# Kernel tuning notes

Measured on AMD Instinct MI355X. Metric: run time of the kernel, lower is better.

Reference implementation:

```python
import jax, jax.numpy as jnp
import numpy as np

T = 50000   # tuple nodes
N = 5000    # base-graph nodes (scatter-mean output size)
E = 800000  # edges per tuple relation
F_IN = 4652
DIM = 256
N_CLASSES = 5


def _lin_init(k, fan_in, fan_out):
    s = 1.0 / np.sqrt(fan_in)
    kw, kb = jax.random.split(k)
    W = jax.random.uniform(kw, (fan_in, fan_out), jnp.float32, -s, s)
    b = jax.random.uniform(kb, (fan_out,), jnp.float32, -s, s)
    return W, b


def setup_inputs() -> dict:
    key = jax.random.key(0)
    ks = jax.random.split(key, 24)
    inp = {}
    inp['x'] = jax.random.normal(ks[0], (T, F_IN), jnp.float32)
    inp['edge_index_1'] = jax.random.randint(ks[1], (2, E), 0, T, jnp.int32)
    inp['edge_index_2'] = jax.random.randint(ks[2], (2, E), 0, T, jnp.int32)
    inp['index_1'] = jax.random.randint(ks[3], (T,), 0, N, jnp.int32)
    inp['index_2'] = jax.random.randint(ks[4], (T,), 0, N, jnp.int32)
    # mlp_init: 4652 -> 256 -> 256
    inp['W_i1'], inp['b_i1'] = _lin_init(ks[5], F_IN, DIM)
    inp['W_i2'], inp['b_i2'] = _lin_init(ks[6], DIM, DIM)
    # GCN convs (PyG GCNConv: weight [in,out], bias [out])
    inp['Wc11'], inp['bc11'] = _lin_init(ks[7], DIM, DIM)
    inp['Wc12'], inp['bc12'] = _lin_init(ks[8], DIM, DIM)
    inp['Wc21'], inp['bc21'] = _lin_init(ks[9], DIM, DIM)
    inp['Wc22'], inp['bc22'] = _lin_init(ks[10], DIM, DIM)
    # mlp_1, mlp_2: 512 -> 256 -> 256
    inp['W_m1a'], inp['b_m1a'] = _lin_init(ks[11], 2 * DIM, DIM)
    inp['W_m1b'], inp['b_m1b'] = _lin_init(ks[12], DIM, DIM)
    inp['W_m2a'], inp['b_m2a'] = _lin_init(ks[13], 2 * DIM, DIM)
    inp['W_m2b'], inp['b_m2b'] = _lin_init(ks[14], DIM, DIM)
    # final mlp: 512 -> 256 -> 5
    inp['W_fa'], inp['b_fa'] = _lin_init(ks[15], 2 * DIM, DIM)
    inp['W_fb'], inp['b_fb'] = _lin_init(ks[16], DIM, N_CLASSES)
    return inp


def _gcn(x, src, dst, W, b):
    # PyG GCNConv default: add self-loops, symmetric deg^-1/2 normalization.
    n = x.shape[0]
    loop = jnp.arange(n, dtype=src.dtype)
    src = jnp.concatenate([src, loop])
    dst = jnp.concatenate([dst, loop])
    deg = jax.ops.segment_sum(jnp.ones_like(dst, x.dtype), dst, num_segments=n)
    dinv = jnp.where(deg > 0, jax.lax.rsqrt(deg), 0.0)
    norm = dinv[src] * dinv[dst]  # [E+n]
    h = x @ W                      # [n, dim]
    agg = jax.ops.segment_sum(h[src] * norm[:, None], dst, num_segments=n)
    return agg + b


def _mlp(x, Wa, ba, Wb, bb):
    return jax.nn.relu(x @ Wa + ba) @ Wb + bb


def _scatter_mean(x, idx, num_segments):
    s = jax.ops.segment_sum(x, idx, num_segments=num_segments)
    c = jax.ops.segment_sum(jnp.ones_like(idx, x.dtype), idx, num_segments=num_segments)
    return s / jnp.maximum(c, 1.0)[:, None]


def reference(x, edge_index_1, edge_index_2, index_1, index_2,
              W_i1, b_i1, W_i2, b_i2,
              Wc11, bc11, Wc12, bc12, Wc21, bc21, Wc22, bc22,
              W_m1a, b_m1a, W_m1b, b_m1b,
              W_m2a, b_m2a, W_m2b, b_m2b,
              W_fa, b_fa, W_fb, b_fb):
    s1, d1 = edge_index_1[0], edge_index_1[1]
    s2, d2 = edge_index_2[0], edge_index_2[1]
    h = _mlp(x, W_i1, b_i1, W_i2, b_i2)
    h1 = jax.nn.relu(_gcn(h, s1, d1, Wc11, bc11))
    h2 = jax.nn.relu(_gcn(h, s2, d2, Wc12, bc12))
    h = _mlp(jnp.concatenate([h1, h2], axis=-1), W_m1a, b_m1a, W_m1b, b_m1b)
    h1 = jax.nn.relu(_gcn(h, s1, d1, Wc21, bc21))
    h2 = jax.nn.relu(_gcn(h, s2, d2, Wc22, bc22))
    h = _mlp(jnp.concatenate([h1, h2], axis=-1), W_m2a, b_m2a, W_m2b, b_m2b)
    r1 = _scatter_mean(h, index_1, N)
    r2 = _scatter_mean(h, index_2, N)
    logits = _mlp(jnp.concatenate([r1, r2], axis=-1), W_fa, b_fa, W_fb, b_fb)
    return jax.nn.log_softmax(logits, axis=1)
```

## Files before the change

### kernel.cpp

```cpp
#include <hip/hip_runtime.h>
#include <hip/hip_bf16.h>

#define T_N 50000
#define N_N 5000
#define E_N 800000
#define FIN 4652
#define KP1 4672
#define DIM 256

typedef __bf16 bf16;
typedef __bf16 bf16x8 __attribute__((ext_vector_type(8)));
typedef float f32x4 __attribute__((ext_vector_type(4)));
typedef unsigned int u32;
typedef __attribute__((address_space(1))) const u32 gu32;
typedef __attribute__((address_space(3))) u32 lu32;

__global__ void prep_w_k(const float* __restrict__ W, bf16* __restrict__ Wt,
                         int K, int Kpad) {
  int k = blockIdx.x;
  int n = threadIdx.x;
  float v = (k < K) ? W[(size_t)k * DIM + n] : 0.f;
  Wt[(size_t)n * Kpad + k] = (bf16)v;
}

__global__ void hist_k(const int* __restrict__ bins, int* __restrict__ cnt, int n) {
  int i = blockIdx.x * 256 + threadIdx.x;
  if (i < n) atomicAdd(&cnt[bins[i]], 1);
}

__global__ void dinv_k(const int* __restrict__ cnt, float* __restrict__ dinv, int n) {
  int i = blockIdx.x * 256 + threadIdx.x;
  if (i < n) dinv[i] = rsqrtf((float)(cnt[i] + 1));
}

__global__ void scan_k(const int* __restrict__ cnt, int* __restrict__ offs,
                       int* __restrict__ curs, int n) {
  __shared__ int wsum[16];
  __shared__ int carry_s;
  int tid = threadIdx.x, wv = tid >> 6, ln = tid & 63;
  if (tid == 0) carry_s = 0;
  __syncthreads();
  for (int base = 0; base < n; base += 1024) {
    int i = base + tid;
    int v = (i < n) ? cnt[i] : 0;
    int s = v;
#pragma unroll
    for (int off = 1; off < 64; off <<= 1) {
      int t = __shfl_up(s, off);
      if (ln >= off) s += t;
    }
    if (ln == 63) wsum[wv] = s;
    __syncthreads();
    if (wv == 0) {
      int w = (ln < 16) ? wsum[ln] : 0;
#pragma unroll
      for (int off = 1; off < 16; off <<= 1) {
        int t = __shfl_up(w, off);
        if (ln >= off) w += t;
      }
      if (ln < 16) wsum[ln] = w;
    }
    __syncthreads();
    int woff = (wv == 0) ? 0 : wsum[wv - 1];
    int total = wsum[15];
    int excl = carry_s + woff + (s - v);
    if (i < n) { offs[i] = excl; curs[i] = excl; }
    __syncthreads();
    if (tid == 0) carry_s += total;
    __syncthreads();
  }
}

__global__ void scatter_k(const int* __restrict__ bins, const int* __restrict__ payload,
                          int* __restrict__ curs, int* __restrict__ out, int n) {
  int i = blockIdx.x * 256 + threadIdx.x;
  if (i < n) {
    int p = atomicAdd(&curs[bins[i]], 1);
    out[p] = payload ? payload[i] : i;
  }
}

__global__ __launch_bounds__(256) void gcn_agg_k(
    const bf16* __restrict__ P, const int* __restrict__ offs,
    const int* __restrict__ cnt, const int* __restrict__ ssrc,
    const float* __restrict__ dinv, const float* __restrict__ bias,
    bf16* __restrict__ HC, int col_off) {
  __shared__ float red[8][256];
  int i = blockIdx.x;
  int tid = threadIdx.x, g = tid >> 5, l = tid & 31;
  float di = dinv[i];
  float acc[8];
#pragma unroll
  for (int j = 0; j < 8; j++) acc[j] = 0.f;
  if (g == 0) {
    bf16x8 v = *(const bf16x8*)(P + (size_t)i * DIM + l * 8);
    float w = di * di;
#pragma unroll
    for (int j = 0; j < 8; j++) acc[j] += (float)v[j] * w;
  }
  int s0 = offs[i], e1 = s0 + cnt[i];
  for (int e = s0 + g; e < e1; e += 8) {
    int s = ssrc[e];
    float w = dinv[s] * di;
    bf16x8 v = *(const bf16x8*)(P + (size_t)s * DIM + l * 8);
#pragma unroll
    for (int j = 0; j < 8; j++) acc[j] += (float)v[j] * w;
  }
#pragma unroll
  for (int j = 0; j < 8; j++) red[g][l * 8 + j] = acc[j];
  __syncthreads();
  float r = 0.f;
#pragma unroll
  for (int gg = 0; gg < 8; gg++) r += red[gg][tid];
  float v = r + bias[tid];
  HC[(size_t)i * 512 + col_off + tid] = (bf16)fmaxf(v, 0.f);
}

__global__ __launch_bounds__(256) void mean_agg_k(
    const bf16* __restrict__ Hf, const int* __restrict__ offs,
    const int* __restrict__ cnt, const int* __restrict__ ids,
    bf16* __restrict__ RC, int col_off) {
  __shared__ float red[8][256];
  int nb = blockIdx.x;
  int tid = threadIdx.x, g = tid >> 5, l = tid & 31;
  int s0 = offs[nb], c = cnt[nb];
  float acc[8];
#pragma unroll
  for (int j = 0; j < 8; j++) acc[j] = 0.f;
  for (int e = s0 + g; e < s0 + c; e += 8) {
    int t = ids[e];
    bf16x8 v = *(const bf16x8*)(Hf + (size_t)t * DIM + l * 8);
#pragma unroll
    for (int j = 0; j < 8; j++) acc[j] += (float)v[j];
  }
#pragma unroll
  for (int j = 0; j < 8; j++) red[g][l * 8 + j] = acc[j];
  __syncthreads();
  float r = 0.f;
#pragma unroll
  for (int gg = 0; gg < 8; gg++) r += red[gg][tid];
  float denom = (c > 0) ? (float)c : 1.f;
  RC[(size_t)nb * 512 + col_off + tid] = (bf16)(r / denom);
}

template <int K>
__global__ __launch_bounds__(256) void gemm_b_k(
    const bf16* __restrict__ A, const bf16* __restrict__ Wt,
    const float* __restrict__ bias, bf16* __restrict__ C,
    int M, int relu) {
  constexpr int RB = K * 2;
  constexpr int RSH = (K == 256) ? 9 : 10;
  constexpr int NC = (64 * RB) / 1024;
  __shared__ __align__(16) char As[64 * RB];
  int tid = threadIdx.x;
  int wv = tid >> 6, ln = tid & 63;
  int q = ln >> 4, r16 = ln & 15;
  int bm = blockIdx.x * 64;
  const char* Ab = (const char*)(A + (size_t)bm * K);
  for (int c = wv; c < NC; c += 4) {
    int lo = c * 1024;
    int t = lo + ln * 16;
    int row = t >> RSH;
    int src = t ^ ((row & 7) << 4);
    __builtin_amdgcn_global_load_lds((gu32*)(Ab + src), (lu32*)(As + lo), 16, 0, 0);
  }
  __syncthreads();

  const bf16* Bp = Wt + (size_t)(wv * 64 + r16) * K + q * 8;
  f32x4 acc[4][4];
#pragma unroll
  for (int i = 0; i < 4; i++)
#pragma unroll
    for (int j = 0; j < 4; j++) acc[i][j] = f32x4{0.f, 0.f, 0.f, 0.f};

  int abase[4], axor[4];
#pragma unroll
  for (int mi = 0; mi < 4; mi++) {
    int row = mi * 16 + r16;
    abase[mi] = row * RB + q * 16;
    axor[mi] = (row & 7) << 4;
  }
#pragma unroll 2
  for (int k0 = 0; k0 < K; k0 += 32) {
    bf16x8 af[4], bv[4];
#pragma unroll
    for (int mi = 0; mi < 4; mi++)
      af[mi] = *(const bf16x8*)(As + ((abase[mi] + k0 * 2) ^ axor[mi]));
#pragma unroll
    for (int ni = 0; ni < 4; ni++)
      bv[ni] = *(const bf16x8*)(Bp + (size_t)ni * 16 * K + k0);
#pragma unroll
    for (int mi = 0; mi < 4; mi++)
#pragma unroll
      for (int ni = 0; ni < 4; ni++)
        acc[mi][ni] = __builtin_amdgcn_mfma_f32_16x16x32_bf16(af[mi], bv[ni], acc[mi][ni], 0, 0, 0);
  }
#pragma unroll
  for (int ni = 0; ni < 4; ni++) {
    int ng = wv * 64 + ni * 16 + r16;
    float bvv = bias ? bias[ng] : 0.f;
#pragma unroll
    for (int mi = 0; mi < 4; mi++) {
#pragma unroll
      for (int rr = 0; rr < 4; rr++) {
        int mg = bm + mi * 16 + q * 4 + rr;
        if (mg < M) {
          float vv = acc[mi][ni][rr] + bvv;
          if (relu) vv = fmaxf(vv, 0.f);
          C[(size_t)mg * DIM + ng] = (bf16)vv;
        }
      }
    }
  }
}

#define LDA 40

__device__ __forceinline__ void load_x8(const float* __restrict__ Xp, int kg, float* f) {
  if (kg + 8 <= FIN) {
    float4 u0 = *(const float4*)(Xp + kg);
    float4 u1 = *(const float4*)(Xp + kg + 4);
    f[0] = u0.x; f[1] = u0.y; f[2] = u0.z; f[3] = u0.w;
    f[4] = u1.x; f[5] = u1.y; f[6] = u1.z; f[7] = u1.w;
  } else {
#pragma unroll
    for (int j = 0; j < 8; j++) f[j] = (kg + j < FIN) ? Xp[kg + j] : 0.f;
  }
}

__global__ __launch_bounds__(256) void gemm_x_k(
    const float* __restrict__ X, const bf16* __restrict__ Wt,
    const float* __restrict__ bias, bf16* __restrict__ C) {
  __shared__ __align__(16) bf16 As[2][64 * LDA];
  int tid = threadIdx.x;
  int wv = tid >> 6, ln = tid & 63;
  int q = ln >> 4, r16 = ln & 15;
  int bm = blockIdx.x * 64;
  int ar = tid >> 2, acol = (tid & 3) * 8;
  int arow = bm + ar; if (arow > T_N - 1) arow = T_N - 1;
  const float* Xp = X + (size_t)arow * FIN;
  const bf16* Bp = Wt + (size_t)(wv * 64 + r16) * KP1 + q * 8;
  f32x4 acc[4][4];
#pragma unroll
  for (int i = 0; i < 4; i++)
#pragma unroll
    for (int j = 0; j < 4; j++) acc[i][j] = f32x4{0.f, 0.f, 0.f, 0.f};

  {
    float f0[8];
    load_x8(Xp, acol, f0);
    bf16x8 av;
#pragma unroll
    for (int j = 0; j < 8; j++) av[j] = (bf16)f0[j];
    *(bf16x8*)&As[0][ar * LDA + acol] = av;
  }
  __syncthreads();
  int cur = 0;
  for (int k0 = 0; k0 < KP1; k0 += 32) {
    float fn[8];
    int have = (k0 + 32 < KP1);
    if (have) load_x8(Xp, k0 + 32 + acol, fn);
    bf16x8 af[4], bv[4];
#pragma unroll
    for (int mi = 0; mi < 4; mi++)
      af[mi] = *(const bf16x8*)&As[cur][(mi * 16 + r16) * LDA + q * 8];
#pragma unroll
    for (int ni = 0; ni < 4; ni++)
      bv[ni] = *(const bf16x8*)(Bp + (size_t)ni * 16 * KP1 + k0);
#pragma unroll
    for (int mi = 0; mi < 4; mi++)
#pragma unroll
      for (int ni = 0; ni < 4; ni++)
        acc[mi][ni] = __builtin_amdgcn_mfma_f32_16x16x32_bf16(af[mi], bv[ni], acc[mi][ni], 0, 0, 0);
    if (have) {
      bf16x8 av;
#pragma unroll
      for (int j = 0; j < 8; j++) av[j] = (bf16)fn[j];
      *(bf16x8*)&As[cur ^ 1][ar * LDA + acol] = av;
    }
    __syncthreads();
    cur ^= 1;
  }
#pragma unroll
  for (int ni = 0; ni < 4; ni++) {
    int ng = wv * 64 + ni * 16 + r16;
    float bv2 = bias[ng];
#pragma unroll
    for (int mi = 0; mi < 4; mi++) {
#pragma unroll
      for (int rr = 0; rr < 4; rr++) {
        int mg = bm + mi * 16 + q * 4 + rr;
        if (mg < T_N) {
          float v = fmaxf(acc[mi][ni][rr] + bv2, 0.f);
          C[(size_t)mg * DIM + ng] = (bf16)v;
        }
      }
    }
  }
}

__global__ void final_k(const bf16* __restrict__ F1, const float* __restrict__ Wfb,
                        const float* __restrict__ bfb, float* __restrict__ out) {
  int i = blockIdx.x, l = threadIdx.x;
  float p[5] = {0.f, 0.f, 0.f, 0.f, 0.f};
  for (int k = l; k < DIM; k += 64) {
    float v = (float)F1[(size_t)i * DIM + k];
#pragma unroll
    for (int c = 0; c < 5; c++) p[c] += v * Wfb[k * 5 + c];
  }
#pragma unroll
  for (int off = 32; off > 0; off >>= 1)
#pragma unroll
    for (int c = 0; c < 5; c++) p[c] += __shfl_down(p[c], off);
  if (l == 0) {
    float z[5], m = -1e30f;
#pragma unroll
    for (int c = 0; c < 5; c++) { z[c] = p[c] + bfb[c]; m = fmaxf(m, z[c]); }
    float s = 0.f;
#pragma unroll
    for (int c = 0; c < 5; c++) s += expf(z[c] - m);
    float ls = m + logf(s);
#pragma unroll
    for (int c = 0; c < 5; c++) out[(size_t)i * 5 + c] = z[c] - ls;
  }
}

extern "C" void kernel_launch(void* const* d_in, const int* in_sizes, int n_in,
                              void* d_out, int out_size, void* d_ws, size_t ws_size,
                              hipStream_t stream) {
  (void)in_sizes; (void)out_size; (void)ws_size;
  if (n_in < 29) return;
  const float* x    = (const float*)d_in[0];
  const int* ei1    = (const int*)d_in[1];
  const int* ei2    = (const int*)d_in[2];
  const int* idx1   = (const int*)d_in[3];
  const int* idx2   = (const int*)d_in[4];
  const float* W_i1 = (const float*)d_in[5];  const float* b_i1 = (const float*)d_in[6];
  const float* W_i2 = (const float*)d_in[7];  const float* b_i2 = (const float*)d_in[8];
  const float* Wc11 = (const float*)d_in[9];  const float* bc11 = (const float*)d_in[10];
  const float* Wc12 = (const float*)d_in[11]; const float* bc12 = (const float*)d_in[12];
  const float* Wc21 = (const float*)d_in[13]; const float* bc21 = (const float*)d_in[14];
  const float* Wc22 = (const float*)d_in[15]; const float* bc22 = (const float*)d_in[16];
  const float* Wm1a = (const float*)d_in[17]; const float* bm1a = (const float*)d_in[18];
  const float* Wm1b = (const float*)d_in[19]; const float* bm1b = (const float*)d_in[20];
  const float* Wm2a = (const float*)d_in[21]; const float* bm2a = (const float*)d_in[22];
  const float* Wm2b = (const float*)d_in[23]; const float* bm2b = (const float*)d_in[24];
  const float* Wfa  = (const float*)d_in[25]; const float* bfa  = (const float*)d_in[26];
  const float* Wfb  = (const float*)d_in[27]; const float* bfb  = (const float*)d_in[28];

  char* base = (char*)d_ws;
  size_t off = 0;
  auto alloc = [&](size_t bytes) -> void* {
    off = (off + 255) & ~(size_t)255;
    void* p = base + off;
    off += bytes;
    return p;
  };

  bf16* WtI1  = (bf16*)alloc((size_t)DIM * KP1 * 2);
  bf16* WtI2  = (bf16*)alloc((size_t)DIM * 256 * 2);
  bf16* WtC11 = (bf16*)alloc((size_t)DIM * 256 * 2);
  bf16* WtC12 = (bf16*)alloc((size_t)DIM * 256 * 2);
  bf16* WtC21 = (bf16*)alloc((size_t)DIM * 256 * 2);
  bf16* WtC22 = (bf16*)alloc((size_t)DIM * 256 * 2);
  bf16* WtM1a = (bf16*)alloc((size_t)DIM * 512 * 2);
  bf16* WtM1b = (bf16*)alloc((size_t)DIM * 256 * 2);
  bf16* WtM2a = (bf16*)alloc((size_t)DIM * 512 * 2);
  bf16* WtM2b = (bf16*)alloc((size_t)DIM * 256 * 2);
  bf16* WtFa  = (bf16*)alloc((size_t)DIM * 512 * 2);

  int* cnt1   = (int*)alloc((size_t)T_N * 4);
  int* cnt2   = (int*)alloc((size_t)T_N * 4);
  int* cntN1  = (int*)alloc((size_t)N_N * 4);
  int* cntN2  = (int*)alloc((size_t)N_N * 4);
  int* offs1  = (int*)alloc((size_t)T_N * 4);
  int* curs1  = (int*)alloc((size_t)T_N * 4);
  int* offs2  = (int*)alloc((size_t)T_N * 4);
  int* curs2  = (int*)alloc((size_t)T_N * 4);
  int* offsN1 = (int*)alloc((size_t)N_N * 4);
  int* cursN1 = (int*)alloc((size_t)N_N * 4);
  int* offsN2 = (int*)alloc((size_t)N_N * 4);
  int* cursN2 = (int*)alloc((size_t)N_N * 4);
  float* dinv1 = (float*)alloc((size_t)T_N * 4);
  float* dinv2 = (float*)alloc((size_t)T_N * 4);
  int* sorted1 = (int*)alloc((size_t)E_N * 4);
  int* sorted2 = (int*)alloc((size_t)E_N * 4);
  int* sortedN1 = (int*)alloc((size_t)T_N * 4);
  int* sortedN2 = (int*)alloc((size_t)T_N * 4);
  bf16* SB0 = (bf16*)alloc((size_t)T_N * DIM * 2);
  bf16* SB1 = (bf16*)alloc((size_t)T_N * DIM * 2);
  bf16* SB2 = (bf16*)alloc((size_t)T_N * 512 * 2);
  bf16* RC  = (bf16*)alloc((size_t)N_N * 512 * 2);
  bf16* F1  = (bf16*)alloc((size_t)N_N * DIM * 2);
  float* out = (float*)d_out;

  hipMemsetAsync(cnt1, 0, (size_t)((char*)cntN2 + (size_t)N_N * 4 - (char*)cnt1), stream);

  prep_w_k<<<KP1, 256, 0, stream>>>(W_i1, WtI1, FIN, KP1);
  prep_w_k<<<256, 256, 0, stream>>>(W_i2, WtI2, 256, 256);
  prep_w_k<<<256, 256, 0, stream>>>(Wc11, WtC11, 256, 256);
  prep_w_k<<<256, 256, 0, stream>>>(Wc12, WtC12, 256, 256);
  prep_w_k<<<256, 256, 0, stream>>>(Wc21, WtC21, 256, 256);
  prep_w_k<<<256, 256, 0, stream>>>(Wc22, WtC22, 256, 256);
  prep_w_k<<<512, 256, 0, stream>>>(Wm1a, WtM1a, 512, 512);
  prep_w_k<<<256, 256, 0, stream>>>(Wm1b, WtM1b, 256, 256);
  prep_w_k<<<512, 256, 0, stream>>>(Wm2a, WtM2a, 512, 512);
  prep_w_k<<<256, 256, 0, stream>>>(Wm2b, WtM2b, 256, 256);
  prep_w_k<<<512, 256, 0, stream>>>(Wfa, WtFa, 512, 512);

  const int GE = (E_N + 255) / 256, GT = (T_N + 255) / 256;
  hist_k<<<GE, 256, 0, stream>>>(ei1 + E_N, cnt1, E_N);
  hist_k<<<GE, 256, 0, stream>>>(ei2 + E_N, cnt2, E_N);
  hist_k<<<GT, 256, 0, stream>>>(idx1, cntN1, T_N);
  hist_k<<<GT, 256, 0, stream>>>(idx2, cntN2, T_N);
  dinv_k<<<GT, 256, 0, stream>>>(cnt1, dinv1, T_N);
  dinv_k<<<GT, 256, 0, stream>>>(cnt2, dinv2, T_N);
  scan_k<<<1, 1024, 0, stream>>>(cnt1, offs1, curs1, T_N);
  scan_k<<<1, 1024, 0, stream>>>(cnt2, offs2, curs2, T_N);
  scan_k<<<1, 1024, 0, stream>>>(cntN1, offsN1, cursN1, N_N);
  scan_k<<<1, 1024, 0, stream>>>(cntN2, offsN2, cursN2, N_N);
  scatter_k<<<GE, 256, 0, stream>>>(ei1 + E_N, ei1, curs1, sorted1, E_N);
  scatter_k<<<GE, 256, 0, stream>>>(ei2 + E_N, ei2, curs2, sorted2, E_N);
  scatter_k<<<GT, 256, 0, stream>>>(idx1, nullptr, cursN1, sortedN1, T_N);
  scatter_k<<<GT, 256, 0, stream>>>(idx2, nullptr, cursN2, sortedN2, T_N);

  const int GM = (T_N + 63) / 64;
  const int GMn = (N_N + 63) / 64;
  gemm_x_k<<<GM, 256, 0, stream>>>(x, WtI1, b_i1, SB0);
  gemm_b_k<256><<<GM, 256, 0, stream>>>(SB0, WtI2, b_i2, SB1, T_N, 0);
  gemm_b_k<256><<<GM, 256, 0, stream>>>(SB1, WtC11, nullptr, SB0, T_N, 0);
  gcn_agg_k<<<T_N, 256, 0, stream>>>(SB0, offs1, cnt1, sorted1, dinv1, bc11, SB2, 0);
  gemm_b_k<256><<<GM, 256, 0, stream>>>(SB1, WtC12, nullptr, SB0, T_N, 0);
  gcn_agg_k<<<T_N, 256, 0, stream>>>(SB0, offs2, cnt2, sorted2, dinv2, bc12, SB2, 256);
  gemm_b_k<512><<<GM, 256, 0, stream>>>(SB2, WtM1a, bm1a, SB1, T_N, 1);
  gemm_b_k<256><<<GM, 256, 0, stream>>>(SB1, WtM1b, bm1b, SB0, T_N, 0);
  gemm_b_k<256><<<GM, 256, 0, stream>>>(SB0, WtC21, nullptr, SB1, T_N, 0);
  gcn_agg_k<<<T_N, 256, 0, stream>>>(SB1, offs1, cnt1, sorted1, dinv1, bc21, SB2, 0);
  gemm_b_k<256><<<GM, 256, 0, stream>>>(SB0, WtC22, nullptr, SB1, T_N, 0);
  gcn_agg_k<<<T_N, 256, 0, stream>>>(SB1, offs2, cnt2, sorted2, dinv2, bc22, SB2, 256);
  gemm_b_k<512><<<GM, 256, 0, stream>>>(SB2, WtM2a, bm2a, SB0, T_N, 1);
  gemm_b_k<256><<<GM, 256, 0, stream>>>(SB0, WtM2b, bm2b, SB1, T_N, 0);
  mean_agg_k<<<N_N, 256, 0, stream>>>(SB1, offsN1, cntN1, sortedN1, RC, 0);
  mean_agg_k<<<N_N, 256, 0, stream>>>(SB1, offsN2, cntN2, sortedN2, RC, 256);
  gemm_b_k<512><<<GMn, 256, 0, stream>>>(RC, WtFa, bfa, F1, N_N, 1);
  final_k<<<N_N, 64, 0, stream>>>(F1, Wfb, bfb, out);
}
```

Baseline: 2.729 ms.

## Batch preprocessing launches and merge paired GCN GEMMs and aggregations

Merges the eleven weight-transpose launches, the four histogram, four scan and four scatter launches into single batched kernels, and folds the dinv computation into the scan. The two per-relation GCN projections now run as one 512-wide GEMM with concatenated weights. The two aggregations and the two scatter-means each become one launch over a 2D grid. This cuts launch count and re-reads of the shared input activation. It adds an extra T×512 buffer and changes the GEMM block size to 512 threads.

```diff
diff --git a/kernel.cpp b/kernel.cpp
--- a/kernel.cpp
+++ b/kernel.cpp
@@ -15,34 +15,55 @@
 typedef __attribute__((address_space(1))) const u32 gu32;
 typedef __attribute__((address_space(3))) u32 lu32;
 
-__global__ void prep_w_k(const float* __restrict__ W, bf16* __restrict__ Wt,
-                         int K, int Kpad) {
-  int k = blockIdx.x;
-  int n = threadIdx.x;
-  float v = (k < K) ? W[(size_t)k * DIM + n] : 0.f;
-  Wt[(size_t)n * Kpad + k] = (bf16)v;
-}
-
-__global__ void hist_k(const int* __restrict__ bins, int* __restrict__ cnt, int n) {
-  int i = blockIdx.x * 256 + threadIdx.x;
-  if (i < n) atomicAdd(&cnt[bins[i]], 1);
-}
-
-__global__ void dinv_k(const int* __restrict__ cnt, float* __restrict__ dinv, int n) {
-  int i = blockIdx.x * 256 + threadIdx.x;
-  if (i < n) dinv[i] = rsqrtf((float)(cnt[i] + 1));
-}
-
-__global__ void scan_k(const int* __restrict__ cnt, int* __restrict__ offs,
-                       int* __restrict__ curs, int n) {
+struct PrepDesc {
+  const float* src[11];
+  bf16* dst[11];
+  int K[11];
+  int off[12];
+};
+
+__global__ void prep_all_k(PrepDesc d) {
+  int b = blockIdx.x, n = threadIdx.x;
+  int e = 0;
+  while (b >= d.off[e + 1]) e++;
+  int k = b - d.off[e];
+  int Kp = d.off[e + 1] - d.off[e];
+  float v = (k < d.K[e]) ? d.src[e][(size_t)k * DIM + n] : 0.f;
+  d.dst[e][(size_t)n * Kp + k] = (bf16)v;
+}
+
+__global__ void hist_all_k(const int* __restrict__ ei1, const int* __restrict__ ei2,
+                           const int* __restrict__ idx1, const int* __restrict__ idx2,
+                           int* __restrict__ cnt1, int* __restrict__ cnt2,
+                           int* __restrict__ cntN1, int* __restrict__ cntN2) {
+  int j = blockIdx.x * 256 + threadIdx.x;
+  if (j < E_N)                    atomicAdd(&cnt1[ei1[E_N + j]], 1);
+  else if (j < 2 * E_N)           atomicAdd(&cnt2[ei2[E_N + (j - E_N)]], 1);
+  else if (j < 2 * E_N + T_N)     atomicAdd(&cntN1[idx1[j - 2 * E_N]], 1);
+  else if (j < 2 * E_N + 2 * T_N) atomicAdd(&cntN2[idx2[j - 2 * E_N - T_N]], 1);
+}
+
+__global__ __launch_bounds__(1024) void scan4_k(
+    const int* __restrict__ c0, const int* __restrict__ c1,
+    const int* __restrict__ c2, const int* __restrict__ c3,
+    int* __restrict__ o0, int* __restrict__ o1, int* __restrict__ o2, int* __restrict__ o3,
+    int* __restrict__ u0, int* __restrict__ u1, int* __restrict__ u2, int* __restrict__ u3,
+    float* __restrict__ dv0, float* __restrict__ dv1) {
   __shared__ int wsum[16];
   __shared__ int carry_s;
+  int b = blockIdx.x;
+  const int* cnt = (b == 0) ? c0 : (b == 1) ? c1 : (b == 2) ? c2 : c3;
+  int* offs = (b == 0) ? o0 : (b == 1) ? o1 : (b == 2) ? o2 : o3;
+  int* curs = (b == 0) ? u0 : (b == 1) ? u1 : (b == 2) ? u2 : u3;
+  float* dv = (b == 0) ? dv0 : (b == 1) ? dv1 : nullptr;
+  int n = (b < 2) ? T_N : N_N;
   int tid = threadIdx.x, wv = tid >> 6, ln = tid & 63;
   if (tid == 0) carry_s = 0;
   __syncthreads();
   for (int base = 0; base < n; base += 1024) {
     int i = base + tid;
     int v = (i < n) ? cnt[i] : 0;
+    if (dv && i < n) dv[i] = rsqrtf((float)(v + 1));
     int s = v;
 #pragma unroll
     for (int off = 1; off < 64; off <<= 1) {
@@ -71,21 +92,43 @@
   }
 }
 
-__global__ void scatter_k(const int* __restrict__ bins, const int* __restrict__ payload,
-                          int* __restrict__ curs, int* __restrict__ out, int n) {
-  int i = blockIdx.x * 256 + threadIdx.x;
-  if (i < n) {
-    int p = atomicAdd(&curs[bins[i]], 1);
-    out[p] = payload ? payload[i] : i;
-  }
-}
-
-__global__ __launch_bounds__(256) void gcn_agg_k(
-    const bf16* __restrict__ P, const int* __restrict__ offs,
-    const int* __restrict__ cnt, const int* __restrict__ ssrc,
-    const float* __restrict__ dinv, const float* __restrict__ bias,
-    bf16* __restrict__ HC, int col_off) {
+__global__ void scatter_all_k(const int* __restrict__ ei1, const int* __restrict__ ei2,
+                              const int* __restrict__ idx1, const int* __restrict__ idx2,
+                              int* __restrict__ u1, int* __restrict__ u2,
+                              int* __restrict__ uN1, int* __restrict__ uN2,
+                              int* __restrict__ s1, int* __restrict__ s2,
+                              int* __restrict__ sN1, int* __restrict__ sN2) {
+  int j = blockIdx.x * 256 + threadIdx.x;
+  if (j < E_N) {
+    int p = atomicAdd(&u1[ei1[E_N + j]], 1); s1[p] = ei1[j];
+  } else if (j < 2 * E_N) {
+    int jj = j - E_N;
+    int p = atomicAdd(&u2[ei2[E_N + jj]], 1); s2[p] = ei2[jj];
+  } else if (j < 2 * E_N + T_N) {
+    int t = j - 2 * E_N;
+    int p = atomicAdd(&uN1[idx1[t]], 1); sN1[p] = t;
+  } else if (j < 2 * E_N + 2 * T_N) {
+    int t = j - 2 * E_N - T_N;
+    int p = atomicAdd(&uN2[idx2[t]], 1); sN2[p] = t;
+  }
+}
+
+__global__ __launch_bounds__(256) void gcn2_k(
+    const bf16* __restrict__ P12,
+    const int* __restrict__ offsA, const int* __restrict__ cntA,
+    const int* __restrict__ srcA, const float* __restrict__ dinvA,
+    const float* __restrict__ biasA,
+    const int* __restrict__ offsB, const int* __restrict__ cntB,
+    const int* __restrict__ srcB, const float* __restrict__ dinvB,
+    const float* __restrict__ biasB,
+    bf16* __restrict__ HC) {
   __shared__ float red[8][256];
+  int y = blockIdx.y;
+  const int* offs = y ? offsB : offsA;
+  const int* cnt  = y ? cntB  : cntA;
+  const int* ssrc = y ? srcB  : srcA;
+  const float* dinv = y ? dinvB : dinvA;
+  const float* bias = y ? biasB : biasA;
   int i = blockIdx.x;
   int tid = threadIdx.x, g = tid >> 5, l = tid & 31;
   float di = dinv[i];
@@ -93,7 +136,7 @@
 #pragma unroll
   for (int j = 0; j < 8; j++) acc[j] = 0.f;
   if (g == 0) {
-    bf16x8 v = *(const bf16x8*)(P + (size_t)i * DIM + l * 8);
+    bf16x8 v = *(const bf16x8*)(P12 + (size_t)i * 512 + y * 256 + l * 8);
     float w = di * di;
 #pragma unroll
     for (int j = 0; j < 8; j++) acc[j] += (float)v[j] * w;
@@ -102,7 +145,7 @@
   for (int e = s0 + g; e < e1; e += 8) {
     int s = ssrc[e];
     float w = dinv[s] * di;
-    bf16x8 v = *(const bf16x8*)(P + (size_t)s * DIM + l * 8);
+    bf16x8 v = *(const bf16x8*)(P12 + (size_t)s * 512 + y * 256 + l * 8);
 #pragma unroll
     for (int j = 0; j < 8; j++) acc[j] += (float)v[j] * w;
   }
@@ -113,14 +156,19 @@
 #pragma unroll
   for (int gg = 0; gg < 8; gg++) r += red[gg][tid];
   float v = r + bias[tid];
-  HC[(size_t)i * 512 + col_off + tid] = (bf16)fmaxf(v, 0.f);
-}
-
-__global__ __launch_bounds__(256) void mean_agg_k(
-    const bf16* __restrict__ Hf, const int* __restrict__ offs,
-    const int* __restrict__ cnt, const int* __restrict__ ids,
-    bf16* __restrict__ RC, int col_off) {
+  HC[(size_t)i * 512 + y * 256 + tid] = (bf16)fmaxf(v, 0.f);
+}
+
+__global__ __launch_bounds__(256) void mean2_k(
+    const bf16* __restrict__ Hf,
+    const int* __restrict__ offsA, const int* __restrict__ cntA, const int* __restrict__ idsA,
+    const int* __restrict__ offsB, const int* __restrict__ cntB, const int* __restrict__ idsB,
+    bf16* __restrict__ RC) {
   __shared__ float red[8][256];
+  int y = blockIdx.y;
+  const int* offs = y ? offsB : offsA;
+  const int* cnt  = y ? cntB  : cntA;
+  const int* ids  = y ? idsB  : idsA;
   int nb = blockIdx.x;
   int tid = threadIdx.x, g = tid >> 5, l = tid & 31;
   int s0 = offs[nb], c = cnt[nb];
@@ -140,24 +188,25 @@
 #pragma unroll
   for (int gg = 0; gg < 8; gg++) r += red[gg][tid];
   float denom = (c > 0) ? (float)c : 1.f;
-  RC[(size_t)nb * 512 + col_off + tid] = (bf16)(r / denom);
-}
-
-template <int K>
-__global__ __launch_bounds__(256) void gemm_b_k(
+  RC[(size_t)nb * 512 + y * 256 + tid] = (bf16)(r / denom);
+}
+
+template <int K, int NOUT>
+__global__ __launch_bounds__(NOUT) void gemm_b_k(
     const bf16* __restrict__ A, const bf16* __restrict__ Wt,
     const float* __restrict__ bias, bf16* __restrict__ C,
     int M, int relu) {
   constexpr int RB = K * 2;
   constexpr int RSH = (K == 256) ? 9 : 10;
   constexpr int NC = (64 * RB) / 1024;
+  constexpr int NW = NOUT / 64;
   __shared__ __align__(16) char As[64 * RB];
   int tid = threadIdx.x;
   int wv = tid >> 6, ln = tid & 63;
   int q = ln >> 4, r16 = ln & 15;
   int bm = blockIdx.x * 64;
   const char* Ab = (const char*)(A + (size_t)bm * K);
-  for (int c = wv; c < NC; c += 4) {
+  for (int c = wv; c < NC; c += NW) {
     int lo = c * 1024;
     int t = lo + ln * 16;
     int row = t >> RSH;
@@ -207,7 +256,7 @@
         if (mg < M) {
           float vv = acc[mi][ni][rr] + bvv;
           if (relu) vv = fmaxf(vv, 0.f);
-          C[(size_t)mg * DIM + ng] = (bf16)vv;
+          C[(size_t)mg * NOUT + ng] = (bf16)vv;
         }
       }
     }
@@ -359,10 +408,8 @@
 
   bf16* WtI1  = (bf16*)alloc((size_t)DIM * KP1 * 2);
   bf16* WtI2  = (bf16*)alloc((size_t)DIM * 256 * 2);
-  bf16* WtC11 = (bf16*)alloc((size_t)DIM * 256 * 2);
-  bf16* WtC12 = (bf16*)alloc((size_t)DIM * 256 * 2);
-  bf16* WtC21 = (bf16*)alloc((size_t)DIM * 256 * 2);
-  bf16* WtC22 = (bf16*)alloc((size_t)DIM * 256 * 2);
+  bf16* WtC1  = (bf16*)alloc((size_t)512 * 256 * 2);
+  bf16* WtC2  = (bf16*)alloc((size_t)512 * 256 * 2);
   bf16* WtM1a = (bf16*)alloc((size_t)DIM * 512 * 2);
   bf16* WtM1b = (bf16*)alloc((size_t)DIM * 256 * 2);
   bf16* WtM2a = (bf16*)alloc((size_t)DIM * 512 * 2);
@@ -389,59 +436,56 @@
   int* sortedN2 = (int*)alloc((size_t)T_N * 4);
   bf16* SB0 = (bf16*)alloc((size_t)T_N * DIM * 2);
   bf16* SB1 = (bf16*)alloc((size_t)T_N * DIM * 2);
-  bf16* SB2 = (bf16*)alloc((size_t)T_N * 512 * 2);
+  bf16* P12 = (bf16*)alloc((size_t)T_N * 512 * 2);
+  bf16* HC  = (bf16*)alloc((size_t)T_N * 512 * 2);
   bf16* RC  = (bf16*)alloc((size_t)N_N * 512 * 2);
   bf16* F1  = (bf16*)alloc((size_t)N_N * DIM * 2);
   float* out = (float*)d_out;
 
   hipMemsetAsync(cnt1, 0, (size_t)((char*)cntN2 + (size_t)N_N * 4 - (char*)cnt1), stream);
 
-  prep_w_k<<<KP1, 256, 0, stream>>>(W_i1, WtI1, FIN, KP1);
-  prep_w_k<<<256, 256, 0, stream>>>(W_i2, WtI2, 256, 256);
-  prep_w_k<<<256, 256, 0, stream>>>(Wc11, WtC11, 256, 256);
-  prep_w_k<<<256, 256, 0, stream>>>(Wc12, WtC12, 256, 256);
-  prep_w_k<<<256, 256, 0, stream>>>(Wc21, WtC21, 256, 256);
-  prep_w_k<<<256, 256, 0, stream>>>(Wc22, WtC22, 256, 256);
-  prep_w_k<<<512, 256, 0, stream>>>(Wm1a, WtM1a, 512, 512);
-  prep_w_k<<<256, 256, 0, stream>>>(Wm1b, WtM1b, 256, 256);
-  prep_w_k<<<512, 256, 0, stream>>>(Wm2a, WtM2a, 512, 512);
-  prep_w_k<<<256, 256, 0, stream>>>(Wm2b, WtM2b, 256, 256);
-  prep_w_k<<<512, 256, 0, stream>>>(Wfa, WtFa, 512, 512);
-
-  const int GE = (E_N + 255) / 256, GT = (T_N + 255) / 256;
-  hist_k<<<GE, 256, 0, stream>>>(ei1 + E_N, cnt1, E_N);
-  hist_k<<<GE, 256, 0, stream>>>(ei2 + E_N, cnt2, E_N);
-  hist_k<<<GT, 256, 0, stream>>>(idx1, cntN1, T_N);
-  hist_k<<<GT, 256, 0, stream>>>(idx2, cntN2, T_N);
-  dinv_k<<<GT, 256, 0, stream>>>(cnt1, dinv1, T_N);
-  dinv_k<<<GT, 256, 0, stream>>>(cnt2, dinv2, T_N);
-  scan_k<<<1, 1024, 0, stream>>>(cnt1, offs1, curs1, T_N);
-  scan_k<<<1, 1024, 0, stream>>>(cnt2, offs2, curs2, T_N);
-  scan_k<<<1, 1024, 0, stream>>>(cntN1, offsN1, cursN1, N_N);
-  scan_k<<<1, 1024, 0, stream>>>(cntN2, offsN2, cursN2, N_N);
-  scatter_k<<<GE, 256, 0, stream>>>(ei1 + E_N, ei1, curs1, sorted1, E_N);
-  scatter_k<<<GE, 256, 0, stream>>>(ei2 + E_N, ei2, curs2, sorted2, E_N);
-  scatter_k<<<GT, 256, 0, stream>>>(idx1, nullptr, cursN1, sortedN1, T_N);
-  scatter_k<<<GT, 256, 0, stream>>>(idx2, nullptr, cursN2, sortedN2, T_N);
+  PrepDesc pp;
+  const float* srcs[11] = {W_i1, W_i2, Wc11, Wc12, Wc21, Wc22, Wm1a, Wm1b, Wm2a, Wm2b, Wfa};
+  bf16* dsts[11] = {WtI1, WtI2, WtC1, WtC1 + (size_t)256 * 256, WtC2, WtC2 + (size_t)256 * 256,
+                    WtM1a, WtM1b, WtM2a, WtM2b, WtFa};
+  int Ks[11] = {FIN, 256, 256, 256, 256, 256, 512, 256, 512, 256, 512};
+  int Kp[11] = {KP1, 256, 256, 256, 256, 256, 512, 256, 512, 256, 512};
+  int acc = 0;
+  for (int e = 0; e < 11; e++) {
+    pp.src[e] = srcs[e]; pp.dst[e] = dsts[e]; pp.K[e] = Ks[e];
+    pp.off[e] = acc; acc += Kp[e];
+  }
+  pp.off[11] = acc;
+  prep_all_k<<<acc, 256, 0, stream>>>(pp);
+
+  const int GP = (2 * E_N + 2 * T_N + 255) / 256;
+  hist_all_k<<<GP, 256, 0, stream>>>(ei1, ei2, idx1, idx2, cnt1, cnt2, cntN1, cntN2);
+  scan4_k<<<4, 1024, 0, stream>>>(cnt1, cnt2, cntN1, cntN2,
+                                  offs1, offs2, offsN1, offsN2,
+                                  curs1, curs2, cursN1, cursN2,
+                                  dinv1, dinv2);
+  scatter_all_k<<<GP, 256, 0, stream>>>(ei1, ei2, idx1, idx2,
+                                        curs1, curs2, cursN1, cursN2,
+                                        sorted1, sorted2, sortedN1, sortedN2);
 
   const int GM = (T_N + 63) / 64;
   const int GMn = (N_N + 63) / 64;
   gemm_x_k<<<GM, 256, 0, stream>>>(x, WtI1, b_i1, SB0);
-  gemm_b_k<256><<<GM, 256, 0, stream>>>(SB0, WtI2, b_i2, SB1, T_N, 0);
-  gemm_b_k<256><<<GM, 256, 0, stream>>>(SB1, WtC11, nullptr, SB0, T_N, 0);
-  gcn_agg_k<<<T_N, 256, 0, stream>>>(SB0, offs1, cnt1, sorted1, dinv1, bc11, SB2, 0);
-  gemm_b_k<256><<<GM, 256, 0, stream>>>(SB1, WtC12, nullptr, SB0, T_N, 0);
-  gcn_agg_k<<<T_N, 256, 0, stream>>>(SB0, offs2, cnt2, sorted2, dinv2, bc12, SB2, 256);
-  gemm_b_k<512><<<GM, 256, 0, stream>>>(SB2, WtM1a, bm1a, SB1, T_N, 1);
-  gemm_b_k<256><<<GM, 256, 0, stream>>>(SB1, WtM1b, bm1b, SB0, T_N, 0);
-  gemm_b_k<256><<<GM, 256, 0, stream>>>(SB0, WtC21, nullptr, SB1, T_N, 0);
-  gcn_agg_k<<<T_N, 256, 0, stream>>>(SB1, offs1, cnt1, sorted1, dinv1, bc21, SB2, 0);
-  gemm_b_k<256><<<GM, 256, 0, stream>>>(SB0, WtC22, nullptr, SB1, T_N, 0);
-  gcn_agg_k<<<T_N, 256, 0, stream>>>(SB1, offs2, cnt2, sorted2, dinv2, bc22, SB2, 256);
-  gemm_b_k<512><<<GM, 256, 0, stream>>>(SB2, WtM2a, bm2a, SB0, T_N, 1);
-  gemm_b_k<256><<<GM, 256, 0, stream>>>(SB0, WtM2b, bm2b, SB1, T_N, 0);
-  mean_agg_k<<<N_N, 256, 0, stream>>>(SB1, offsN1, cntN1, sortedN1, RC, 0);
-  mean_agg_k<<<N_N, 256, 0, stream>>>(SB1, offsN2, cntN2, sortedN2, RC, 256);
-  gemm_b_k<512><<<GMn, 256, 0, stream>>>(RC, WtFa, bfa, F1, N_N, 1);
+  gemm_b_k<256, 256><<<GM, 256, 0, stream>>>(SB0, WtI2, b_i2, SB1, T_N, 0);
+  gemm_b_k<256, 512><<<GM, 512, 0, stream>>>(SB1, WtC1, nullptr, P12, T_N, 0);
+  gcn2_k<<<dim3(T_N, 2), 256, 0, stream>>>(P12,
+      offs1, cnt1, sorted1, dinv1, bc11,
+      offs2, cnt2, sorted2, dinv2, bc12, HC);
+  gemm_b_k<512, 256><<<GM, 256, 0, stream>>>(HC, WtM1a, bm1a, SB0, T_N, 1);
+  gemm_b_k<256, 256><<<GM, 256, 0, stream>>>(SB0, WtM1b, bm1b, SB1, T_N, 0);
+  gemm_b_k<256, 512><<<GM, 512, 0, stream>>>(SB1, WtC2, nullptr, P12, T_N, 0);
+  gcn2_k<<<dim3(T_N, 2), 256, 0, stream>>>(P12,
+      offs1, cnt1, sorted1, dinv1, bc21,
+      offs2, cnt2, sorted2, dinv2, bc22, HC);
+  gemm_b_k<512, 256><<<GM, 256, 0, stream>>>(HC, WtM2a, bm2a, SB0, T_N, 1);
+  gemm_b_k<256, 256><<<GM, 256, 0, stream>>>(SB0, WtM2b, bm2b, SB1, T_N, 0);
+  mean2_k<<<dim3(N_N, 2), 256, 0, stream>>>(SB1,
+      offsN1, cntN1, sortedN1, offsN2, cntN2, sortedN2, RC);
+  gemm_b_k<512, 256><<<GMn, 256, 0, stream>>>(RC, WtFa, bfa, F1, N_N, 1);
   final_k<<<N_N, 64, 0, stream>>>(F1, Wfb, bfb, out);
 }
```

Measured after the change: 2.604 ms. -4.6%, faster.
